# Kernel optimization log

Hardware: AMD Instinct MI355X
Metric: run time of the kernel (lower is better)

The kernel has to match this reference:

```python
import jax, jax.numpy as jnp
import numpy as np

T, B, LAG, H = 128, 1024, 6, 256


def setup_inputs() -> dict:
    key = jax.random.key(0)
    ks = jax.random.split(key, 16)
    s = 0.05  # small init scale to keep LSTM gates in a sane range
    d = {}
    d["x"] = jax.random.normal(ks[0], (T, B, LAG), jnp.float32)
    d["Wi1"] = jax.random.normal(ks[1], (H, LAG), jnp.float32) * s
    d["bi1"] = jnp.zeros((H,), jnp.float32)
    d["Wi2"] = jax.random.normal(ks[2], (H, H), jnp.float32) * s
    d["bi2"] = jnp.zeros((H,), jnp.float32)
    d["Wi3"] = jax.random.normal(ks[3], (H, H), jnp.float32) * s
    d["bi3"] = jnp.zeros((H,), jnp.float32)
    d["Wih0"] = jax.random.normal(ks[4], (4 * H, H), jnp.float32) * s
    d["Whh0"] = jax.random.normal(ks[5], (4 * H, H), jnp.float32) * s
    d["bih0"] = jnp.zeros((4 * H,), jnp.float32)
    d["bhh0"] = jnp.zeros((4 * H,), jnp.float32)
    d["Wih1"] = jax.random.normal(ks[6], (4 * H, H), jnp.float32) * s
    d["Whh1"] = jax.random.normal(ks[7], (4 * H, H), jnp.float32) * s
    d["bih1"] = jnp.zeros((4 * H,), jnp.float32)
    d["bhh1"] = jnp.zeros((4 * H,), jnp.float32)
    d["Wo1"] = jax.random.normal(ks[8], (H, H), jnp.float32) * s
    d["bo1"] = jnp.zeros((H,), jnp.float32)
    d["Wo2"] = jax.random.normal(ks[9], (H, H), jnp.float32) * s
    d["bo2"] = jnp.zeros((H,), jnp.float32)
    d["Wo3"] = jax.random.normal(ks[10], (LAG, H), jnp.float32) * s
    d["bo3"] = jnp.zeros((LAG,), jnp.float32)
    return d


def _lstm_cell(xt, h, c, Wih, Whh, bih, bhh):
    # PyTorch gate order: i, f, g, o
    g = xt @ Wih.T + h @ Whh.T + (bih + bhh)
    i, f, gg, o = jnp.split(g, 4, axis=-1)
    c2 = jax.nn.sigmoid(f) * c + jax.nn.sigmoid(i) * jnp.tanh(gg)
    h2 = jax.nn.sigmoid(o) * jnp.tanh(c2)
    return h2, c2


def reference(x, Wi1, bi1, Wi2, bi2, Wi3, bi3,
              Wih0, Whh0, bih0, bhh0, Wih1, Whh1, bih1, bhh1,
              Wo1, bo1, Wo2, bo2, Wo3, bo3):
    relu = jax.nn.relu
    # input MLP applied to every timestep at once: [T,B,6] -> [T,B,H]
    u = relu(x @ Wi1.T + bi1)
    u = relu(u @ Wi2.T + bi2)
    u = relu(u @ Wi3.T + bi3)

    def step(carry, xt):
        h0, c0, h1, c1 = carry
        h0, c0 = _lstm_cell(xt, h0, c0, Wih0, Whh0, bih0, bhh0)
        # dropout(0.05) between layers is identity in eval mode
        h1, c1 = _lstm_cell(h0, h1, c1, Wih1, Whh1, bih1, bhh1)
        return (h0, c0, h1, c1), h1

    z = jnp.zeros((x.shape[1], Whh0.shape[1]), x.dtype)
    _, hs = jax.lax.scan(step, (z, z, z, z), u)  # hs: [T,B,H]

    # output MLP: ReLU, Linear, ReLU, Linear, ReLU, Linear(H->6)
    y = relu(hs)
    y = relu(y @ Wo1.T + bo1)
    y = relu(y @ Wo2.T + bo2)
    y = y @ Wo3.T + bo3
    return y  # [T,B,6]
```

## Files before the change

kernel.cpp:

```cpp
#include <hip/hip_runtime.h>
#include <math.h>


namespace {
constexpr int kT   = 128;
constexpr int kB   = 1024;
constexpr int kLag = 6;
constexpr int kH   = 256;
constexpr int kTc  = 32;
constexpr int kMc  = kTc * kB;
constexpr int kGS  = 68;
constexpr int kLdsBytes = 2 * 32768 + 2 * 64 * kGS * 4;
constexpr int kRankMain = 4096;
constexpr int kCntUints = 16384;
}

typedef _Float16 half8 __attribute__((ext_vector_type(8)));
typedef _Float16 half4 __attribute__((ext_vector_type(4)));
typedef float f32x4 __attribute__((ext_vector_type(4)));
typedef unsigned long long u64;

__device__ __forceinline__ float sigm(float x) {
    return 1.f / (1.f + exp2f(-1.4426950408889634f * x));
}
__device__ __forceinline__ float tanh_(float x) {
    return 2.f / (1.f + exp2f(-2.8853900817779268f * x)) - 1.f;
}

__device__ __forceinline__ half8 pack(u64 a, u64 b) {
    union { u64 u[2]; half8 h; } r;
    r.u[0] = a; r.u[1] = b;
    return r.h;
}

__device__ __forceinline__ void ld_l2(half8& d, const _Float16* p) {
    asm volatile("global_load_dwordx4 %0, %1, off sc0"
                 : "=v"(d) : "v"(p) : "memory");
}
#define WAITCNT_HOLD8(A, B)                                                   \
    asm volatile("s_waitcnt vmcnt(0)"                                         \
        : "+v"(A[0]), "+v"(A[1]), "+v"(A[2]), "+v"(A[3]),                     \
          "+v"(B[0]), "+v"(B[1]), "+v"(B[2]), "+v"(B[3]))

__global__ __launch_bounds__(256)
void zero_fill(unsigned int* __restrict__ p)
{
    p[blockIdx.x * 256 + threadIdx.x] = 0u;
}

__global__ __launch_bounds__(256)
void cvt_f2h(const float* __restrict__ s, _Float16* __restrict__ d)
{
    const int i = blockIdx.x * 256 + threadIdx.x;
    d[i] = (_Float16)s[i];
}

__global__ __launch_bounds__(256)
void build_wcat2(const float* __restrict__ Wih, const float* __restrict__ Whh,
                 _Float16* __restrict__ d)
{
    const int i = blockIdx.x * 256 + threadIdx.x;
    const int row = i >> 9, col = i & 511;
    const int js = row >> 6, r6 = row & 63;
    const int tt = r6 >> 4, e = r6 & 15;
    const int c = e >> 2, g = e & 3;
    const int src = g * 256 + js * 16 + tt * 4 + c;
    const float v = (col < 256) ? Wih[src * 256 + col] : Whh[src * 256 + col - 256];
    d[i] = (_Float16)v;
}

__global__ __launch_bounds__(256)
void add_bias(const float* __restrict__ a, const float* __restrict__ b,
              float* __restrict__ d)
{
    const int i = blockIdx.x * 256 + threadIdx.x;
    d[i] = a[i] + b[i];
}

__global__ __launch_bounds__(256)
void in_mlp1(const float* __restrict__ x, const float* __restrict__ Wi1,
             const float* __restrict__ bi1, _Float16* __restrict__ out)
{
    const int idx = blockIdx.x * 256 + threadIdx.x;
    const int col = idx & (kH - 1);
    const int row = idx >> 8;
    const float* xr = x + (size_t)row * kLag;
    const float* w  = Wi1 + col * kLag;
    float s = bi1[col];
#pragma unroll
    for (int k = 0; k < kLag; ++k) s = fmaf(xr[k], w[k], s);
    out[idx] = (_Float16)fmaxf(s, 0.f);
}

__global__ __launch_bounds__(256)
void gemm_h16(const _Float16* __restrict__ A, const _Float16* __restrict__ W,
              const float* __restrict__ bias, _Float16* __restrict__ C)
{
    const int tid = threadIdx.x;
    const int w = tid >> 6, lane = tid & 63, q = lane >> 4, l15 = lane & 15;
    const int n0 = blockIdx.x * 64;
    const int r0 = blockIdx.y * 128 + w * 32;

    half8 bf[4][8];
#pragma unroll
    for (int nt = 0; nt < 4; ++nt)
#pragma unroll
        for (int kk = 0; kk < 8; ++kk)
            bf[nt][kk] = *(const half8*)(W + (size_t)(n0 + nt * 16 + l15) * 256
                                         + kk * 32 + q * 8);
    float bz[4];
#pragma unroll
    for (int nt = 0; nt < 4; ++nt) bz[nt] = bias[n0 + nt * 16 + l15];

#pragma unroll
    for (int rt = 0; rt < 2; ++rt) {
        const _Float16* arow = A + (size_t)(r0 + rt * 16 + l15) * 256 + q * 8;
        half8 af[8];
#pragma unroll
        for (int kk = 0; kk < 8; ++kk) af[kk] = *(const half8*)(arow + kk * 32);
        f32x4 acc[4];
#pragma unroll
        for (int nt = 0; nt < 4; ++nt)
            acc[nt] = (f32x4){bz[nt], bz[nt], bz[nt], bz[nt]};
#pragma unroll
        for (int kk = 0; kk < 8; ++kk)
#pragma unroll
            for (int nt = 0; nt < 4; ++nt)
                acc[nt] = __builtin_amdgcn_mfma_f32_16x16x32_f16(
                    af[kk], bf[nt][kk], acc[nt], 0, 0, 0);
#pragma unroll
        for (int nt = 0; nt < 4; ++nt)
#pragma unroll
            for (int r = 0; r < 4; ++r) {
                const float v = fmaxf(acc[nt][r], 0.f);
                C[(size_t)(r0 + rt * 16 + q * 4 + r) * 256 + n0 + nt * 16 + l15]
                    = (_Float16)v;
            }
    }
}

__device__ __forceinline__ void waitpeers(const unsigned int* __restrict__ fb,
                                          unsigned int target, int tid)
{
    if (tid < 64) {
        const unsigned int* fp = fb + (tid & 15) * 16;
        unsigned int v;
        do {
            v = __hip_atomic_load(fp, __ATOMIC_RELAXED,
                                  __HIP_MEMORY_SCOPE_AGENT);
        } while (__any(v < target));
    }
    __syncthreads();
}

__device__ __forceinline__ void gather_lo(const _Float16* lo, int row, int q,
                                          u64* ua)
{
    const u64* plo = (const u64*)(lo + (size_t)row * 256 + q * 8);
#pragma unroll
    for (int kk = 0; kk < 8; ++kk) {
        ua[2*kk]   = plo[kk*8];
        ua[2*kk+1] = plo[kk*8 + 1];
    }
}

__device__ __forceinline__ void gstore(float* __restrict__ gl, int m0, int nb,
                                       int q, int l15,
                                       const f32x4& a0, const f32x4& a1)
{
#pragma unroll
    for (int r = 0; r < 4; ++r) {
        gl[(m0 + q*4 + r) * kGS + nb + l15]      = a0[r];
        gl[(m0 + q*4 + r) * kGS + nb + 16 + l15] = a1[r];
    }
}

__device__ __forceinline__ void phase_gemm_lds2(
    const char* pA, const char* pB,
    const half8 (&B0)[16], const half8 (&B1)[16],
    float* __restrict__ gl, int rtb, int nb, int q, int l15)
{
#pragma unroll
    for (int rt = 0; rt < 2; ++rt) {
        const int row = (rtb + rt) * 16 + l15;
        const int xr  = ((row & 15) << 4) ^ ((row & 1) << 8);
        const int rb  = row * 512;
        f32x4 a0 = {0.f,0.f,0.f,0.f}, a1 = {0.f,0.f,0.f,0.f};
#pragma unroll
        for (int kk = 0; kk < 8; ++kk) {
            const int off = rb + ((q * 16 + kk * 64) ^ xr);
            const half8 alo = *(const half8*)(pA + off);
            const half8 ahi = *(const half8*)(pB + off);
            a0 = __builtin_amdgcn_mfma_f32_16x16x32_f16(alo, B0[kk],     a0, 0,0,0);
            a1 = __builtin_amdgcn_mfma_f32_16x16x32_f16(alo, B1[kk],     a1, 0,0,0);
            a0 = __builtin_amdgcn_mfma_f32_16x16x32_f16(ahi, B0[8 + kk], a0, 0,0,0);
            a1 = __builtin_amdgcn_mfma_f32_16x16x32_f16(ahi, B1[8 + kk], a1, 0,0,0);
        }
        gstore(gl, (rtb + rt) * 16, nb, q, l15, a0, a1);
    }
}

__device__ __forceinline__ void phase_gemm_l0(
    const _Float16* __restrict__ u, const char* pH0,
    const half8 (&B0)[16], const half8 (&B1)[16],
    float* __restrict__ gl, int rtb, int nb, int q, int l15)
{
    half8 uf[2][8];
#pragma unroll
    for (int rt = 0; rt < 2; ++rt) {
        const _Float16* pu = u + (size_t)((rtb + rt) * 16 + l15) * 256 + q * 8;
#pragma unroll
        for (int kk = 0; kk < 8; ++kk)
            uf[rt][kk] = *(const half8*)(pu + kk * 32);
    }
#pragma unroll
    for (int rt = 0; rt < 2; ++rt) {
        const int row = (rtb + rt) * 16 + l15;
        const int xr  = ((row & 15) << 4) ^ ((row & 1) << 8);
        const int rb  = row * 512;
        f32x4 a0 = {0.f,0.f,0.f,0.f}, a1 = {0.f,0.f,0.f,0.f};
#pragma unroll
        for (int kk = 0; kk < 8; ++kk) {
            const int off = rb + ((q * 16 + kk * 64) ^ xr);
            const half8 ah = *(const half8*)(pH0 + off);
            a0 = __builtin_amdgcn_mfma_f32_16x16x32_f16(uf[rt][kk], B0[kk], a0, 0,0,0);
            a1 = __builtin_amdgcn_mfma_f32_16x16x32_f16(uf[rt][kk], B1[kk], a1, 0,0,0);
            a0 = __builtin_amdgcn_mfma_f32_16x16x32_f16(ah, B0[8 + kk],     a0, 0,0,0);
            a1 = __builtin_amdgcn_mfma_f32_16x16x32_f16(ah, B1[8 + kk],     a1, 0,0,0);
        }
        gstore(gl, (rtb + rt) * 16, nb, q, l15, a0, a1);
    }
}

__device__ __forceinline__ void cells_wave(const float* __restrict__ gl,
    int grow, int hclb, const float* __restrict__ bs, float* __restrict__ cst,
    _Float16* __restrict__ hout, _Float16* __restrict__ uout)
{
    const float* gr = gl + grow * kGS + hclb * 4;
    half4 hv;
#pragma unroll
    for (int c = 0; c < 4; ++c) {
        const f32x4 g4 = *(const f32x4*)(gr + c * 4);
        const float gi = g4[0] + bs[c*4 + 0];
        const float gf = g4[1] + bs[c*4 + 1];
        const float gg = g4[2] + bs[c*4 + 2];
        const float go = g4[3] + bs[c*4 + 3];
        const float c2 = sigm(gf) * cst[c] + sigm(gi) * tanh_(gg);
        cst[c] = c2;
        hv[c] = (_Float16)(sigm(go) * tanh_(c2));
    }
    *(half4*)(hout + (size_t)grow * 256 + hclb) = hv;
    if (uout) {
        const _Float16 z = (_Float16)0.f;
        half4 uv;
#pragma unroll
        for (int c = 0; c < 4; ++c) uv[c] = hv[c] > z ? hv[c] : z;
        *(half4*)(uout + (size_t)grow * 256 + hclb) = uv;
    }
}

__global__ __launch_bounds__(512, 2)
void lstm_all(_Float16* __restrict__ ubuf,
              const _Float16* __restrict__ Wc0, const _Float16* __restrict__ Wc1,
              const float* __restrict__ bc0, const float* __restrict__ bc1,
              _Float16* __restrict__ h0b, _Float16* __restrict__ h1b,
              unsigned int* __restrict__ cnt)
{
    extern __shared__ char lds[];
    char* pH0  = lds;
    char* pH1  = lds + 32768;
    float* gl0 = (float*)(lds + 65536);
    float* gl1 = gl0 + 64 * kGS;

    const int tid = threadIdx.x;
    const int w = tid >> 6, lane = tid & 63, q = lane >> 4, l15 = lane & 15;
    const int wl = w & 3;
    const int rtb = (wl >> 1) * 2;
    const int nbw = wl & 1;
    const int nb  = nbw * 32;
    const int lyr = (w < 4) ? 1 : 0;

    __shared__ int sh_bi, sh_js;
    if (tid == 0) {
        unsigned int xcd = __builtin_amdgcn_s_getreg(20 | (31 << 11)) & 7u;
        unsigned int rank = __hip_atomic_fetch_add(cnt + kRankMain + xcd * 16, 1u,
            __ATOMIC_RELAXED, __HIP_MEMORY_SCOPE_AGENT);
        sh_bi = (int)(xcd * 2 + (rank >> 4));
        sh_js = (int)(rank & 15);
    }
    __syncthreads();
    const int bi = sh_bi, js = sh_js;
    unsigned int* fb    = cnt + (size_t)bi * 256;
    unsigned int* fslot = fb + js * 16;

    const _Float16* WcL = lyr ? Wc1 : Wc0;
    half8 Bf0[16], Bf1[16];
    {
        const _Float16* wr0 = WcL
            + (size_t)(js * 64 + (nbw * 2    ) * 16 + l15) * 512 + q * 8;
        const _Float16* wr1 = WcL
            + (size_t)(js * 64 + (nbw * 2 + 1) * 16 + l15) * 512 + q * 8;
#pragma unroll
        for (int kk = 0; kk < 16; ++kk) {
            Bf0[kk] = *(const half8*)(wr0 + kk * 32);
            Bf1[kk] = *(const half8*)(wr1 + kk * 32);
        }
    }

    int sdst[4];
#pragma unroll
    for (int r = 0; r < 4; ++r) {
        const int L   = tid * 16 + r * 8192;
        const int row = L >> 9;
        const int c   = L & 511;
        sdst[r] = row * 512 + (c ^ ((row & 15) << 4) ^ ((row & 1) << 8));
    }

    const int grow = rtb * 16 + (lane >> 1);
    const int hclb = nbw * 8 + (lane & 1) * 4;
    const float* bcL = lyr ? bc1 : bc0;
    float bs[16];
#pragma unroll
    for (int c = 0; c < 4; ++c)
#pragma unroll
        for (int g = 0; g < 4; ++g)
            bs[c*4 + g] = bcL[g * 256 + js * 16 + hclb + c];
    float cst[4] = {0.f, 0.f, 0.f, 0.f};
    const size_t rbase = (size_t)bi * 64 * 256;
    const size_t hoff  = rbase + js * 16;

    if (lyr == 0) {
#pragma unroll
        for (int rt = 0; rt < 2; ++rt) {
            u64 ua[16];
            gather_lo(ubuf + rbase, (rtb + rt) * 16 + l15, q, ua);
            f32x4 a0 = {0.f,0.f,0.f,0.f}, a1 = {0.f,0.f,0.f,0.f};
#pragma unroll
            for (int kk = 0; kk < 8; ++kk) {
                const half8 af = pack(ua[2*kk], ua[2*kk+1]);
                a0 = __builtin_amdgcn_mfma_f32_16x16x32_f16(af, Bf0[kk], a0, 0,0,0);
                a1 = __builtin_amdgcn_mfma_f32_16x16x32_f16(af, Bf1[kk], a1, 0,0,0);
            }
            gstore(gl0, (rtb + rt) * 16, nb, q, l15, a0, a1);
        }
        cells_wave(gl0, grow, hclb, bs, cst, (_Float16*)(h0b + hoff), nullptr);
    }
    asm volatile("s_waitcnt vmcnt(0)" ::: "memory");
    __syncthreads();
    if (tid == 0)
        __hip_atomic_fetch_add(fslot, 1u, __ATOMIC_RELAXED,
                               __HIP_MEMORY_SCOPE_AGENT);

    for (int t = 0; t < kT; ++t) {
        const size_t p  = (size_t)(t & 1) * kB * 256;
        const size_t pn = (size_t)((t & 1) ^ 1) * kB * 256;
        const bool hasB = (t < kT - 1);

        waitpeers(fb, (unsigned)(t + 1), tid);

        {
            half8 s0[4], s1h[4];
            const char* b0 = (const char*)(h0b + p  + rbase);
            const char* b1 = (const char*)(h1b + pn + rbase);
#pragma unroll
            for (int r = 0; r < 4; ++r) {
                ld_l2(s0[r],  (const _Float16*)(b0 + tid * 16 + r * 8192));
                ld_l2(s1h[r], (const _Float16*)(b1 + tid * 16 + r * 8192));
            }
            WAITCNT_HOLD8(s0, s1h);
#pragma unroll
            for (int r = 0; r < 4; ++r) {
                *(half8*)(pH0 + sdst[r]) = s0[r];
                *(half8*)(pH1 + sdst[r]) = s1h[r];
            }
        }
        __syncthreads();

        if (lyr == 1) {
            phase_gemm_lds2(pH0, pH1, Bf0, Bf1, gl1, rtb, nb, q, l15);
            cells_wave(gl1, grow, hclb, bs, cst,
                       (_Float16*)(h1b + p + hoff),
                       (_Float16*)(ubuf + (size_t)t * kB * 256 + hoff));
        } else if (hasB) {
            phase_gemm_l0(ubuf + (size_t)(t + 1) * kB * 256 + rbase, pH0,
                          Bf0, Bf1, gl0, rtb, nb, q, l15);
            cells_wave(gl0, grow, hclb, bs, cst,
                       (_Float16*)(h0b + pn + hoff), nullptr);
        }

        asm volatile("s_waitcnt vmcnt(0)" ::: "memory");
        __syncthreads();
        if (hasB && tid == 0)
            __hip_atomic_fetch_add(fslot, 1u, __ATOMIC_RELAXED,
                                   __HIP_MEMORY_SCOPE_AGENT);
    }
}

__global__ __launch_bounds__(256)
void out_mlp3(const _Float16* __restrict__ y2, const float* __restrict__ Wo3,
              const float* __restrict__ bo3, float* __restrict__ out)
{
    const int lane = threadIdx.x & 63;
    const int row  = blockIdx.x * 4 + (threadIdx.x >> 6);
    const _Float16* yr = y2 + (size_t)row * kH + lane * 4;
    const float a0 = (float)yr[0], a1 = (float)yr[1], a2 = (float)yr[2], a3 = (float)yr[3];
    float s[kLag];
#pragma unroll
    for (int o = 0; o < kLag; ++o) {
        const float4 wv = *(const float4*)(Wo3 + o * kH + lane * 4);
        s[o] = a0 * wv.x + a1 * wv.y + a2 * wv.z + a3 * wv.w;
    }
#pragma unroll
    for (int off = 32; off > 0; off >>= 1) {
#pragma unroll
        for (int o = 0; o < kLag; ++o) s[o] += __shfl_down(s[o], off);
    }
    if (lane == 0) {
#pragma unroll
        for (int o = 0; o < kLag; ++o)
            out[(size_t)row * kLag + o] = s[o] + bo3[o];
    }
}

extern "C" void kernel_launch(void* const* d_in, const int* in_sizes, int n_in,
                              void* d_out, int out_size, void* d_ws, size_t ws_size,
                              hipStream_t stream)
{
    const float* x    = (const float*)d_in[0];
    const float* Wi1  = (const float*)d_in[1];
    const float* bi1  = (const float*)d_in[2];
    const float* Wi2  = (const float*)d_in[3];
    const float* bi2  = (const float*)d_in[4];
    const float* Wi3  = (const float*)d_in[5];
    const float* bi3  = (const float*)d_in[6];
    const float* Wih0 = (const float*)d_in[7];
    const float* Whh0 = (const float*)d_in[8];
    const float* bih0 = (const float*)d_in[9];
    const float* bhh0 = (const float*)d_in[10];
    const float* Wih1 = (const float*)d_in[11];
    const float* Whh1 = (const float*)d_in[12];
    const float* bih1 = (const float*)d_in[13];
    const float* bhh1 = (const float*)d_in[14];
    const float* Wo1  = (const float*)d_in[15];
    const float* bo1  = (const float*)d_in[16];
    const float* Wo2  = (const float*)d_in[17];
    const float* bo2  = (const float*)d_in[18];
    const float* Wo3  = (const float*)d_in[19];
    const float* bo3  = (const float*)d_in[20];
    float* outp = (float*)d_out;

    char* p = (char*)d_ws;
    _Float16* ubuf = (_Float16*)p;  p += (size_t)kT * kB * kH * 2;
    _Float16* s1   = (_Float16*)p;  p += (size_t)kMc * kH * 2;
    _Float16* s2   = (_Float16*)p;  p += (size_t)kMc * kH * 2;
    _Float16* Wc0  = (_Float16*)p;  p += (size_t)1024 * 512 * 2;
    _Float16* Wc1  = (_Float16*)p;  p += (size_t)1024 * 512 * 2;
    _Float16* W2h  = (_Float16*)p;  p += (size_t)kH * kH * 2;
    _Float16* W3h  = (_Float16*)p;  p += (size_t)kH * kH * 2;
    _Float16* Wo1h = (_Float16*)p;  p += (size_t)kH * kH * 2;
    _Float16* Wo2h = (_Float16*)p;  p += (size_t)kH * kH * 2;
    float* bc0 = (float*)p;  p += 1024 * 4;
    float* bc1 = (float*)p;  p += 1024 * 4;
    _Float16* h0b = (_Float16*)p;  p += (size_t)2 * kB * kH * 2;
    _Float16* h1b = (_Float16*)p;  p += (size_t)2 * kB * kH * 2;
    unsigned int* cnt = (unsigned int*)p;  p += kCntUints * 4;

    zero_fill<<<2112, 256, 0, stream>>>((unsigned int*)h0b);
    cvt_f2h<<<kH * kH / 256, 256, 0, stream>>>(Wi2, W2h);
    cvt_f2h<<<kH * kH / 256, 256, 0, stream>>>(Wi3, W3h);
    cvt_f2h<<<kH * kH / 256, 256, 0, stream>>>(Wo1, Wo1h);
    cvt_f2h<<<kH * kH / 256, 256, 0, stream>>>(Wo2, Wo2h);
    build_wcat2<<<1024 * 512 / 256, 256, 0, stream>>>(Wih0, Whh0, Wc0);
    build_wcat2<<<1024 * 512 / 256, 256, 0, stream>>>(Wih1, Whh1, Wc1);
    add_bias<<<4, 256, 0, stream>>>(bih0, bhh0, bc0);
    add_bias<<<4, 256, 0, stream>>>(bih1, bhh1, bc1);

    for (int c = 0; c < kT / kTc; ++c) {
        in_mlp1<<<kMc * kH / 256, 256, 0, stream>>>(
            x + (size_t)c * kMc * kLag, Wi1, bi1, s1);
        gemm_h16<<<dim3(4, kMc / 128), 256, 0, stream>>>(s1, W2h, bi2, s2);
        gemm_h16<<<dim3(4, kMc / 128), 256, 0, stream>>>(
            s2, W3h, bi3, ubuf + (size_t)c * kMc * kH);
    }

    static bool attr_set = false;
    if (!attr_set) {
        hipFuncSetAttribute((const void*)lstm_all,
                            hipFuncAttributeMaxDynamicSharedMemorySize, kLdsBytes);
        attr_set = true;
    }
    void* args[] = {&ubuf, &Wc0, &Wc1, &bc0, &bc1, &h0b, &h1b, &cnt};
    hipLaunchCooperativeKernel((const void*)lstm_all, dim3(256), dim3(512),
                               args, kLdsBytes, stream);

    for (int c = 0; c < kT / kTc; ++c) {
        gemm_h16<<<dim3(4, kMc / 128), 256, 0, stream>>>(
            ubuf + (size_t)c * kMc * kH, Wo1h, bo1, s1);
        gemm_h16<<<dim3(4, kMc / 128), 256, 0, stream>>>(s1, Wo2h, bo2, s2);
        out_mlp3<<<kMc / 4, 256, 0, stream>>>(
            s2, Wo3, bo3, outp + (size_t)c * kMc * kLag);
    }
}
```

Before: 2.031 ms.

## Repartition LSTM blocks to 32 batch rows and hoist input GEMM before peer wait

Changes the persistent LSTM decomposition so each block handles 32 batch rows by 128 gate columns, with 8 column-blocks per batch group instead of 16. That is fewer peers to poll and a smaller hidden-state gather per step. Weight packing is changed to a simple gate-interleaved order to match. The layer-0 input projection for the next timestep is now computed before waiting on peers, so it overlaps the synchronization latency. LDS use is forced up to 96KB, which limits occupancy to one block per CU but matches the cooperative grid of 256 blocks.

```diff
diff --git a/kernel.cpp b/kernel.cpp
--- a/kernel.cpp
+++ b/kernel.cpp
@@ -9,8 +9,8 @@
 constexpr int kH   = 256;
 constexpr int kTc  = 32;
 constexpr int kMc  = kTc * kB;
-constexpr int kGS  = 68;
-constexpr int kLdsBytes = 2 * 32768 + 2 * 64 * kGS * 4;
+constexpr int kGS  = 132;
+constexpr int kLdsForce = 98304;
 constexpr int kRankMain = 4096;
 constexpr int kCntUints = 16384;
 }
@@ -37,10 +37,9 @@
     asm volatile("global_load_dwordx4 %0, %1, off sc0"
                  : "=v"(d) : "v"(p) : "memory");
 }
-#define WAITCNT_HOLD8(A, B)                                                   \
+#define WAITCNT_HOLD4(A, B)                                                   \
     asm volatile("s_waitcnt vmcnt(0)"                                         \
-        : "+v"(A[0]), "+v"(A[1]), "+v"(A[2]), "+v"(A[3]),                     \
-          "+v"(B[0]), "+v"(B[1]), "+v"(B[2]), "+v"(B[3]))
+        : "+v"(A[0]), "+v"(A[1]), "+v"(B[0]), "+v"(B[1]))
 
 __global__ __launch_bounds__(256)
 void zero_fill(unsigned int* __restrict__ p)
@@ -56,15 +55,12 @@
 }
 
 __global__ __launch_bounds__(256)
-void build_wcat2(const float* __restrict__ Wih, const float* __restrict__ Whh,
+void build_wcat3(const float* __restrict__ Wih, const float* __restrict__ Whh,
                  _Float16* __restrict__ d)
 {
     const int i = blockIdx.x * 256 + threadIdx.x;
     const int row = i >> 9, col = i & 511;
-    const int js = row >> 6, r6 = row & 63;
-    const int tt = r6 >> 4, e = r6 & 15;
-    const int c = e >> 2, g = e & 3;
-    const int src = g * 256 + js * 16 + tt * 4 + c;
+    const int src = (row & 3) * 256 + (row >> 2);
     const float v = (col < 256) ? Wih[src * 256 + col] : Whh[src * 256 + col - 256];
     d[i] = (_Float16)v;
 }
@@ -143,7 +139,7 @@
                                           unsigned int target, int tid)
 {
     if (tid < 64) {
-        const unsigned int* fp = fb + (tid & 15) * 16;
+        const unsigned int* fp = fb + (tid & 7) * 16;
         unsigned int v;
         do {
             v = __hip_atomic_load(fp, __ATOMIC_RELAXED,
@@ -164,79 +160,22 @@
     }
 }
 
-__device__ __forceinline__ void gstore(float* __restrict__ gl, int m0, int nb,
+__device__ __forceinline__ void gstore(float* __restrict__ gl, int rt, int wl,
                                        int q, int l15,
                                        const f32x4& a0, const f32x4& a1)
 {
 #pragma unroll
     for (int r = 0; r < 4; ++r) {
-        gl[(m0 + q*4 + r) * kGS + nb + l15]      = a0[r];
-        gl[(m0 + q*4 + r) * kGS + nb + 16 + l15] = a1[r];
-    }
-}
-
-__device__ __forceinline__ void phase_gemm_lds2(
-    const char* pA, const char* pB,
-    const half8 (&B0)[16], const half8 (&B1)[16],
-    float* __restrict__ gl, int rtb, int nb, int q, int l15)
-{
-#pragma unroll
-    for (int rt = 0; rt < 2; ++rt) {
-        const int row = (rtb + rt) * 16 + l15;
-        const int xr  = ((row & 15) << 4) ^ ((row & 1) << 8);
-        const int rb  = row * 512;
-        f32x4 a0 = {0.f,0.f,0.f,0.f}, a1 = {0.f,0.f,0.f,0.f};
-#pragma unroll
-        for (int kk = 0; kk < 8; ++kk) {
-            const int off = rb + ((q * 16 + kk * 64) ^ xr);
-            const half8 alo = *(const half8*)(pA + off);
-            const half8 ahi = *(const half8*)(pB + off);
-            a0 = __builtin_amdgcn_mfma_f32_16x16x32_f16(alo, B0[kk],     a0, 0,0,0);
-            a1 = __builtin_amdgcn_mfma_f32_16x16x32_f16(alo, B1[kk],     a1, 0,0,0);
-            a0 = __builtin_amdgcn_mfma_f32_16x16x32_f16(ahi, B0[8 + kk], a0, 0,0,0);
-            a1 = __builtin_amdgcn_mfma_f32_16x16x32_f16(ahi, B1[8 + kk], a1, 0,0,0);
-        }
-        gstore(gl, (rtb + rt) * 16, nb, q, l15, a0, a1);
-    }
-}
-
-__device__ __forceinline__ void phase_gemm_l0(
-    const _Float16* __restrict__ u, const char* pH0,
-    const half8 (&B0)[16], const half8 (&B1)[16],
-    float* __restrict__ gl, int rtb, int nb, int q, int l15)
-{
-    half8 uf[2][8];
-#pragma unroll
-    for (int rt = 0; rt < 2; ++rt) {
-        const _Float16* pu = u + (size_t)((rtb + rt) * 16 + l15) * 256 + q * 8;
-#pragma unroll
-        for (int kk = 0; kk < 8; ++kk)
-            uf[rt][kk] = *(const half8*)(pu + kk * 32);
-    }
-#pragma unroll
-    for (int rt = 0; rt < 2; ++rt) {
-        const int row = (rtb + rt) * 16 + l15;
-        const int xr  = ((row & 15) << 4) ^ ((row & 1) << 8);
-        const int rb  = row * 512;
-        f32x4 a0 = {0.f,0.f,0.f,0.f}, a1 = {0.f,0.f,0.f,0.f};
-#pragma unroll
-        for (int kk = 0; kk < 8; ++kk) {
-            const int off = rb + ((q * 16 + kk * 64) ^ xr);
-            const half8 ah = *(const half8*)(pH0 + off);
-            a0 = __builtin_amdgcn_mfma_f32_16x16x32_f16(uf[rt][kk], B0[kk], a0, 0,0,0);
-            a1 = __builtin_amdgcn_mfma_f32_16x16x32_f16(uf[rt][kk], B1[kk], a1, 0,0,0);
-            a0 = __builtin_amdgcn_mfma_f32_16x16x32_f16(ah, B0[8 + kk],     a0, 0,0,0);
-            a1 = __builtin_amdgcn_mfma_f32_16x16x32_f16(ah, B1[8 + kk],     a1, 0,0,0);
-        }
-        gstore(gl, (rtb + rt) * 16, nb, q, l15, a0, a1);
+        gl[(rt*16 + q*4 + r) * kGS + wl*32 + l15]      = a0[r];
+        gl[(rt*16 + q*4 + r) * kGS + wl*32 + 16 + l15] = a1[r];
     }
 }
 
 __device__ __forceinline__ void cells_wave(const float* __restrict__ gl,
-    int grow, int hclb, const float* __restrict__ bs, float* __restrict__ cst,
+    int grow, int gcb, const float* __restrict__ bs, float* __restrict__ cst,
     _Float16* __restrict__ hout, _Float16* __restrict__ uout)
 {
-    const float* gr = gl + grow * kGS + hclb * 4;
+    const float* gr = gl + grow * kGS + gcb;
     half4 hv;
 #pragma unroll
     for (int c = 0; c < 4; ++c) {
@@ -249,13 +188,13 @@
         cst[c] = c2;
         hv[c] = (_Float16)(sigm(go) * tanh_(c2));
     }
-    *(half4*)(hout + (size_t)grow * 256 + hclb) = hv;
+    *(half4*)hout = hv;
     if (uout) {
         const _Float16 z = (_Float16)0.f;
         half4 uv;
 #pragma unroll
         for (int c = 0; c < 4; ++c) uv[c] = hv[c] > z ? hv[c] : z;
-        *(half4*)(uout + (size_t)grow * 256 + hclb) = uv;
+        *(half4*)uout = uv;
     }
 }
 
@@ -268,16 +207,13 @@
 {
     extern __shared__ char lds[];
     char* pH0  = lds;
-    char* pH1  = lds + 32768;
-    float* gl0 = (float*)(lds + 65536);
-    float* gl1 = gl0 + 64 * kGS;
+    char* pH1  = lds + 16384;
+    float* gl0 = (float*)(lds + 32768);
+    float* gl1 = gl0 + 32 * kGS;
 
     const int tid = threadIdx.x;
     const int w = tid >> 6, lane = tid & 63, q = lane >> 4, l15 = lane & 15;
     const int wl = w & 3;
-    const int rtb = (wl >> 1) * 2;
-    const int nbw = wl & 1;
-    const int nb  = nbw * 32;
     const int lyr = (w < 4) ? 1 : 0;
 
     __shared__ int sh_bi, sh_js;
@@ -285,21 +221,19 @@
         unsigned int xcd = __builtin_amdgcn_s_getreg(20 | (31 << 11)) & 7u;
         unsigned int rank = __hip_atomic_fetch_add(cnt + kRankMain + xcd * 16, 1u,
             __ATOMIC_RELAXED, __HIP_MEMORY_SCOPE_AGENT);
-        sh_bi = (int)(xcd * 2 + (rank >> 4));
-        sh_js = (int)(rank & 15);
+        sh_bi = (int)(xcd * 4 + (rank >> 3));
+        sh_js = (int)(rank & 7);
     }
     __syncthreads();
     const int bi = sh_bi, js = sh_js;
-    unsigned int* fb    = cnt + (size_t)bi * 256;
+    unsigned int* fb    = cnt + (size_t)bi * 128;
     unsigned int* fslot = fb + js * 16;
 
     const _Float16* WcL = lyr ? Wc1 : Wc0;
     half8 Bf0[16], Bf1[16];
     {
-        const _Float16* wr0 = WcL
-            + (size_t)(js * 64 + (nbw * 2    ) * 16 + l15) * 512 + q * 8;
-        const _Float16* wr1 = WcL
-            + (size_t)(js * 64 + (nbw * 2 + 1) * 16 + l15) * 512 + q * 8;
+        const _Float16* wr0 = WcL + (size_t)(js*128 + wl*32 + l15) * 512 + q * 8;
+        const _Float16* wr1 = wr0 + (size_t)16 * 512;
 #pragma unroll
         for (int kk = 0; kk < 16; ++kk) {
             Bf0[kk] = *(const half8*)(wr0 + kk * 32);
@@ -307,33 +241,34 @@
         }
     }
 
-    int sdst[4];
-#pragma unroll
-    for (int r = 0; r < 4; ++r) {
+    int sdst[2];
+#pragma unroll
+    for (int r = 0; r < 2; ++r) {
         const int L   = tid * 16 + r * 8192;
         const int row = L >> 9;
         const int c   = L & 511;
         sdst[r] = row * 512 + (c ^ ((row & 15) << 4) ^ ((row & 1) << 8));
     }
 
-    const int grow = rtb * 16 + (lane >> 1);
-    const int hclb = nbw * 8 + (lane & 1) * 4;
+    const int grow = lane >> 1;
+    const int gcb  = wl*32 + (lane & 1) * 16;
+    const int hcb  = js*32 + wl*8 + (lane & 1) * 4;
     const float* bcL = lyr ? bc1 : bc0;
     float bs[16];
 #pragma unroll
     for (int c = 0; c < 4; ++c)
 #pragma unroll
         for (int g = 0; g < 4; ++g)
-            bs[c*4 + g] = bcL[g * 256 + js * 16 + hclb + c];
+            bs[c*4 + g] = bcL[g * 256 + hcb + c];
     float cst[4] = {0.f, 0.f, 0.f, 0.f};
-    const size_t rbase = (size_t)bi * 64 * 256;
-    const size_t hoff  = rbase + js * 16;
+    const size_t rbase = (size_t)bi * 32 * 256;
+    const size_t coff  = rbase + (size_t)grow * 256 + hcb;
 
     if (lyr == 0) {
 #pragma unroll
         for (int rt = 0; rt < 2; ++rt) {
             u64 ua[16];
-            gather_lo(ubuf + rbase, (rtb + rt) * 16 + l15, q, ua);
+            gather_lo(ubuf + rbase, rt*16 + l15, q, ua);
             f32x4 a0 = {0.f,0.f,0.f,0.f}, a1 = {0.f,0.f,0.f,0.f};
 #pragma unroll
             for (int kk = 0; kk < 8; ++kk) {
@@ -341,9 +276,9 @@
                 a0 = __builtin_amdgcn_mfma_f32_16x16x32_f16(af, Bf0[kk], a0, 0,0,0);
                 a1 = __builtin_amdgcn_mfma_f32_16x16x32_f16(af, Bf1[kk], a1, 0,0,0);
             }
-            gstore(gl0, (rtb + rt) * 16, nb, q, l15, a0, a1);
+            gstore(gl0, rt, wl, q, l15, a0, a1);
         }
-        cells_wave(gl0, grow, hclb, bs, cst, (_Float16*)(h0b + hoff), nullptr);
+        cells_wave(gl0, grow, gcb, bs, cst, (_Float16*)(h0b + coff), nullptr);
     }
     asm volatile("s_waitcnt vmcnt(0)" ::: "memory");
     __syncthreads();
@@ -356,20 +291,48 @@
         const size_t pn = (size_t)((t & 1) ^ 1) * kB * 256;
         const bool hasB = (t < kT - 1);
 
+        f32x4 aA0 = {0.f,0.f,0.f,0.f}, aA1 = {0.f,0.f,0.f,0.f};
+        f32x4 aB0 = {0.f,0.f,0.f,0.f}, aB1 = {0.f,0.f,0.f,0.f};
+        if (lyr == 0 && hasB) {
+            const _Float16* u = ubuf + (size_t)(t + 1) * kB * 256 + rbase;
+            {
+                const _Float16* pu = u + (size_t)(l15) * 256 + q * 8;
+                half8 uf[8];
+#pragma unroll
+                for (int kk = 0; kk < 8; ++kk) uf[kk] = *(const half8*)(pu + kk * 32);
+#pragma unroll
+                for (int kk = 0; kk < 8; ++kk) {
+                    aA0 = __builtin_amdgcn_mfma_f32_16x16x32_f16(uf[kk], Bf0[kk], aA0, 0,0,0);
+                    aA1 = __builtin_amdgcn_mfma_f32_16x16x32_f16(uf[kk], Bf1[kk], aA1, 0,0,0);
+                }
+            }
+            {
+                const _Float16* pu = u + (size_t)(16 + l15) * 256 + q * 8;
+                half8 uf[8];
+#pragma unroll
+                for (int kk = 0; kk < 8; ++kk) uf[kk] = *(const half8*)(pu + kk * 32);
+#pragma unroll
+                for (int kk = 0; kk < 8; ++kk) {
+                    aB0 = __builtin_amdgcn_mfma_f32_16x16x32_f16(uf[kk], Bf0[kk], aB0, 0,0,0);
+                    aB1 = __builtin_amdgcn_mfma_f32_16x16x32_f16(uf[kk], Bf1[kk], aB1, 0,0,0);
+                }
+            }
+        }
+
         waitpeers(fb, (unsigned)(t + 1), tid);
 
         {
-            half8 s0[4], s1h[4];
+            half8 s0[2], s1h[2];
             const char* b0 = (const char*)(h0b + p  + rbase);
             const char* b1 = (const char*)(h1b + pn + rbase);
 #pragma unroll
-            for (int r = 0; r < 4; ++r) {
+            for (int r = 0; r < 2; ++r) {
                 ld_l2(s0[r],  (const _Float16*)(b0 + tid * 16 + r * 8192));
                 ld_l2(s1h[r], (const _Float16*)(b1 + tid * 16 + r * 8192));
             }
-            WAITCNT_HOLD8(s0, s1h);
-#pragma unroll
-            for (int r = 0; r < 4; ++r) {
+            WAITCNT_HOLD4(s0, s1h);
+#pragma unroll
+            for (int r = 0; r < 2; ++r) {
                 *(half8*)(pH0 + sdst[r]) = s0[r];
                 *(half8*)(pH1 + sdst[r]) = s1h[r];
             }
@@ -377,15 +340,56 @@
         __syncthreads();
 
         if (lyr == 1) {
-            phase_gemm_lds2(pH0, pH1, Bf0, Bf1, gl1, rtb, nb, q, l15);
-            cells_wave(gl1, grow, hclb, bs, cst,
-                       (_Float16*)(h1b + p + hoff),
-                       (_Float16*)(ubuf + (size_t)t * kB * 256 + hoff));
+#pragma unroll
+            for (int rt = 0; rt < 2; ++rt) {
+                const int row = rt*16 + l15;
+                const int xr  = ((row & 15) << 4) ^ ((row & 1) << 8);
+                const int rb  = row * 512;
+                f32x4 a0 = {0.f,0.f,0.f,0.f}, a1 = {0.f,0.f,0.f,0.f};
+#pragma unroll
+                for (int kk = 0; kk < 8; ++kk) {
+                    const int off = rb + ((q * 16 + kk * 64) ^ xr);
+                    const half8 alo = *(const half8*)(pH0 + off);
+                    const half8 ahi = *(const half8*)(pH1 + off);
+                    a0 = __builtin_amdgcn_mfma_f32_16x16x32_f16(alo, Bf0[kk],     a0, 0,0,0);
+                    a1 = __builtin_amdgcn_mfma_f32_16x16x32_f16(alo, Bf1[kk],     a1, 0,0,0);
+                    a0 = __builtin_amdgcn_mfma_f32_16x16x32_f16(ahi, Bf0[8 + kk], a0, 0,0,0);
+                    a1 = __builtin_amdgcn_mfma_f32_16x16x32_f16(ahi, Bf1[8 + kk], a1, 0,0,0);
+                }
+                gstore(gl1, rt, wl, q, l15, a0, a1);
+            }
+            cells_wave(gl1, grow, gcb, bs, cst,
+                       (_Float16*)(h1b + p + coff),
+                       (_Float16*)(ubuf + (size_t)t * kB * 256 + coff));
         } else if (hasB) {
-            phase_gemm_l0(ubuf + (size_t)(t + 1) * kB * 256 + rbase, pH0,
-                          Bf0, Bf1, gl0, rtb, nb, q, l15);
-            cells_wave(gl0, grow, hclb, bs, cst,
-                       (_Float16*)(h0b + pn + hoff), nullptr);
+            {
+                const int row = l15;
+                const int xr  = ((row & 15) << 4) ^ ((row & 1) << 8);
+                const int rb  = row * 512;
+#pragma unroll
+                for (int kk = 0; kk < 8; ++kk) {
+                    const int off = rb + ((q * 16 + kk * 64) ^ xr);
+                    const half8 ah = *(const half8*)(pH0 + off);
+                    aA0 = __builtin_amdgcn_mfma_f32_16x16x32_f16(ah, Bf0[8 + kk], aA0, 0,0,0);
+                    aA1 = __builtin_amdgcn_mfma_f32_16x16x32_f16(ah, Bf1[8 + kk], aA1, 0,0,0);
+                }
+                gstore(gl0, 0, wl, q, l15, aA0, aA1);
+            }
+            {
+                const int row = 16 + l15;
+                const int xr  = ((row & 15) << 4) ^ ((row & 1) << 8);
+                const int rb  = row * 512;
+#pragma unroll
+                for (int kk = 0; kk < 8; ++kk) {
+                    const int off = rb + ((q * 16 + kk * 64) ^ xr);
+                    const half8 ah = *(const half8*)(pH0 + off);
+                    aB0 = __builtin_amdgcn_mfma_f32_16x16x32_f16(ah, Bf0[8 + kk], aB0, 0,0,0);
+                    aB1 = __builtin_amdgcn_mfma_f32_16x16x32_f16(ah, Bf1[8 + kk], aB1, 0,0,0);
+                }
+                gstore(gl0, 1, wl, q, l15, aB0, aB1);
+            }
+            cells_wave(gl0, grow, gcb, bs, cst,
+                       (_Float16*)(h0b + pn + coff), nullptr);
         }
 
         asm volatile("s_waitcnt vmcnt(0)" ::: "memory");
@@ -470,8 +474,8 @@
     cvt_f2h<<<kH * kH / 256, 256, 0, stream>>>(Wi3, W3h);
     cvt_f2h<<<kH * kH / 256, 256, 0, stream>>>(Wo1, Wo1h);
     cvt_f2h<<<kH * kH / 256, 256, 0, stream>>>(Wo2, Wo2h);
-    build_wcat2<<<1024 * 512 / 256, 256, 0, stream>>>(Wih0, Whh0, Wc0);
-    build_wcat2<<<1024 * 512 / 256, 256, 0, stream>>>(Wih1, Whh1, Wc1);
+    build_wcat3<<<1024 * 512 / 256, 256, 0, stream>>>(Wih0, Whh0, Wc0);
+    build_wcat3<<<1024 * 512 / 256, 256, 0, stream>>>(Wih1, Whh1, Wc1);
     add_bias<<<4, 256, 0, stream>>>(bih0, bhh0, bc0);
     add_bias<<<4, 256, 0, stream>>>(bih1, bhh1, bc1);
 
@@ -486,12 +490,12 @@
     static bool attr_set = false;
     if (!attr_set) {
         hipFuncSetAttribute((const void*)lstm_all,
-                            hipFuncAttributeMaxDynamicSharedMemorySize, kLdsBytes);
+                            hipFuncAttributeMaxDynamicSharedMemorySize, kLdsForce);
         attr_set = true;
     }
     void* args[] = {&ubuf, &Wc0, &Wc1, &bc0, &bc1, &h0b, &h1b, &cnt};
     hipLaunchCooperativeKernel((const void*)lstm_all, dim3(256), dim3(512),
-                               args, kLdsBytes, stream);
+                               args, kLdsForce, stream);
 
     for (int c = 0; c < kT / kTc; ++c) {
         gemm_h16<<<dim3(4, kMc / 128), 256, 0, stream>>>(
```

New measurement: 2.091 ms. +3.0%, slower.
